# Performance work log

Measured on AMD Instinct MI355X. Metric: run time of the kernel, lower is better.

The kernel has to match this reference:

```python
import jax, jax.numpy as jnp
import numpy as np

D_MODEL = 512
D_FF = 512
N_EXPERTS = 16
TOP_K = 3
BATCH, SEQ = 1, 2048


def setup_inputs() -> dict:
    key = jax.random.key(0)
    ks = jax.random.split(key, 6)
    x = jax.random.normal(ks[0], (BATCH, SEQ, D_MODEL), dtype=jnp.float32)
    # router gate (std=0.01 per _init_weights)
    gate_w = 0.01 * jax.random.normal(ks[1], (N_EXPERTS, D_MODEL), dtype=jnp.float32)
    expert_bias = jnp.zeros((N_EXPERTS,), dtype=jnp.float32)  # registered buffer, zeros
    # shared SwiGLU expert (std=0.02)
    shared_gate_up = 0.02 * jax.random.normal(ks[2], (2 * D_FF, D_MODEL), dtype=jnp.float32)
    shared_down = 0.02 * jax.random.normal(ks[3], (D_MODEL, D_FF), dtype=jnp.float32)
    # batched routed experts (std=0.02)
    expert_gate_up = 0.02 * jax.random.normal(ks[4], (N_EXPERTS, 2 * D_FF, D_MODEL), dtype=jnp.float32)
    expert_down = 0.02 * jax.random.normal(ks[5], (N_EXPERTS, D_MODEL, D_FF), dtype=jnp.float32)
    return {
        "x": x,
        "gate_w": gate_w,
        "expert_bias": expert_bias,
        "shared_gate_up": shared_gate_up,
        "shared_down": shared_down,
        "expert_gate_up": expert_gate_up,
        "expert_down": expert_down,
    }


def _swiglu(combined):
    gate, up = jnp.split(combined, 2, axis=-1)
    return jax.nn.silu(gate) * up


def reference(x, gate_w, expert_bias, shared_gate_up, shared_down, expert_gate_up, expert_down):
    B, S, D = x.shape
    xf = x.reshape(-1, D)  # [T, D]

    # ---- shared expert (always active) ----
    shared_out = _swiglu(xf @ shared_gate_up.T) @ shared_down.T  # [T, D]

    # ---- router: sigmoid affinity + bias-adjusted top-k ----
    logits = xf @ gate_w.T  # [T, E]
    affinity = jax.nn.sigmoid(logits)
    routing_scores = affinity + expert_bias  # expert_bias buffer (zeros)
    _, sel = jax.lax.top_k(routing_scores, TOP_K)  # [T, K]
    sel_aff = jnp.take_along_axis(affinity, sel, axis=1)  # [T, K]
    gating = sel_aff / (sel_aff.sum(axis=-1, keepdims=True) + 1e-9)  # [T, K]

    # ---- routed experts: per-token SwiGLU with the token's expert weights ----
    # Computed densely per expert then gathered; identical math to the
    # per-token weight-gather in BatchedExperts.
    combined = jnp.einsum('td,efd->tef', xf, expert_gate_up)  # [T, E, 2F]
    hidden = _swiglu(combined)  # [T, E, F]
    expert_out = jnp.einsum('tef,edf->ted', hidden, expert_down)  # [T, E, D]
    sel_out = jnp.take_along_axis(expert_out, sel[:, :, None], axis=1)  # [T, K, D]
    routed_out = jnp.einsum('tk,tkd->td', gating, sel_out)  # [T, D]

    out = shared_out + routed_out  # dropout p=0.0 -> identity
    return out.reshape(B, S, D)
```

## Files before the change

kernel.cpp:

```cpp
#include <hip/hip_runtime.h>

#define T_TOK 2048
#define DM    512
#define DFF   512
#define NE    16
#define LDK   72

typedef __attribute__((ext_vector_type(8))) short bf16x8;
typedef __attribute__((ext_vector_type(4))) float f32x4;
typedef __attribute__((ext_vector_type(8))) unsigned short us8;

__device__ __forceinline__ unsigned short f2bf(float f) {
  unsigned int u = __float_as_uint(f);
  u += 0x7fffu + ((u >> 16) & 1u);
  return (unsigned short)(u >> 16);
}

__device__ __forceinline__ void cvt16(const float* __restrict__ p, us8* o) {
  float4 v0 = *(const float4*)(p);
  float4 v1 = *(const float4*)(p + 4);
  float4 v2 = *(const float4*)(p + 8);
  float4 v3 = *(const float4*)(p + 12);
  us8 a, b;
  a[0]=f2bf(v0.x); a[1]=f2bf(v0.y); a[2]=f2bf(v0.z); a[3]=f2bf(v0.w);
  a[4]=f2bf(v1.x); a[5]=f2bf(v1.y); a[6]=f2bf(v1.z); a[7]=f2bf(v1.w);
  b[0]=f2bf(v2.x); b[1]=f2bf(v2.y); b[2]=f2bf(v2.z); b[3]=f2bf(v2.w);
  b[4]=f2bf(v3.x); b[5]=f2bf(v3.y); b[6]=f2bf(v3.z); b[7]=f2bf(v3.w);
  o[0]=a; o[1]=b;
}

template<bool PRE>
__device__ __forceinline__ void stage16(const void* __restrict__ base, size_t off, us8* o) {
  if constexpr (PRE) {
    const unsigned short* p = (const unsigned short*)base + off;
    o[0] = *(const us8*)p;
    o[1] = *(const us8*)(p + 8);
  } else {
    cvt16((const float*)base + off, o);
  }
}

#define MFMA(a,b,c) __builtin_amdgcn_mfma_f32_16x16x32_bf16((a),(b),(c),0,0,0)

__global__ __launch_bounds__(256) void router_kernel(
    const float* __restrict__ x, const float* __restrict__ gw,
    const float* __restrict__ bias, int* __restrict__ counts,
    int* __restrict__ list, float* __restrict__ wgt)
{
  __shared__ float lg[4][16];
  __shared__ int bcnt[16], bbase[16];
  __shared__ int sel_s[4][3], pos_s[4][3];
  __shared__ float g_s[4][3];

  const int tid = threadIdx.x, w = tid >> 6, lane = tid & 63;
  if (tid < 16) bcnt[tid] = 0;
  const int tok = blockIdx.x * 4 + w;
  const int e = lane & 15, part = lane >> 4;

  const float* xr = x + (size_t)tok * DM + part * 128;
  const float* wr = gw + (size_t)e * DM + part * 128;
  float acc = 0.f;
  #pragma unroll 8
  for (int i = 0; i < 128; i += 4) {
    float4 xv = *(const float4*)(xr + i);
    float4 wv = *(const float4*)(wr + i);
    acc += xv.x*wv.x + xv.y*wv.y + xv.z*wv.z + xv.w*wv.w;
  }
  acc += __shfl_xor(acc, 16);
  acc += __shfl_xor(acc, 32);
  if (lane < 16) lg[w][lane] = 1.f / (1.f + __expf(-acc));
  __syncthreads();

  if (tid < 4) {
    float aff[16], sc[16];
    #pragma unroll
    for (int i = 0; i < 16; ++i) { aff[i] = lg[tid][i]; sc[i] = aff[i] + bias[i]; }
    int sel[3]; float sa[3]; float sum = 0.f;
    #pragma unroll
    for (int k = 0; k < 3; ++k) {
      float best = -1e30f; int bi = 0;
      for (int i = 0; i < 16; ++i) {
        bool used = false;
        for (int j = 0; j < k; ++j) used |= (sel[j] == i);
        if (!used && sc[i] > best) { best = sc[i]; bi = i; }
      }
      sel[k] = bi; sa[k] = aff[bi]; sum += aff[bi];
    }
    float inv = 1.f / (sum + 1e-9f);
    #pragma unroll
    for (int k = 0; k < 3; ++k) {
      int p = atomicAdd(&bcnt[sel[k]], 1);
      sel_s[tid][k] = sel[k]; pos_s[tid][k] = p; g_s[tid][k] = sa[k] * inv;
    }
  }
  __syncthreads();
  if (tid < 16) bbase[tid] = atomicAdd(&counts[tid], bcnt[tid]);
  __syncthreads();
  if (tid < 4) {
    #pragma unroll
    for (int k = 0; k < 3; ++k) {
      int E = sel_s[tid][k];
      int p = bbase[E] + pos_s[tid][k];
      list[E * T_TOK + p] = blockIdx.x * 4 + tid;
      wgt [E * T_TOK + p] = g_s[tid][k];
    }
  }
}

__global__ __launch_bounds__(256) void conv_kernel(
    const float* __restrict__ x,   const float* __restrict__ sgu,
    const float* __restrict__ sdn, const float* __restrict__ egu,
    const float* __restrict__ edn,
    unsigned short* __restrict__ xb,   unsigned short* __restrict__ sgub,
    unsigned short* __restrict__ sdnb, unsigned short* __restrict__ egub,
    unsigned short* __restrict__ ednb)
{
  int g = blockIdx.x * 256 + threadIdx.x;
  const float* s; unsigned short* d; int l;
  if      (g <  131072) { s = x;   d = xb;   l = g;           }
  else if (g <  196608) { s = sgu; d = sgub; l = g -  131072; }
  else if (g <  229376) { s = sdn; d = sdnb; l = g -  196608; }
  else if (g < 1277952) { s = egu; d = egub; l = g -  229376; }
  else                  { s = edn; d = ednb; l = g - 1277952; }
  const float* p = s + (size_t)l * 8;
  float4 v0 = *(const float4*)p;
  float4 v1 = *(const float4*)(p + 4);
  us8 o;
  o[0]=f2bf(v0.x); o[1]=f2bf(v0.y); o[2]=f2bf(v0.z); o[3]=f2bf(v0.w);
  o[4]=f2bf(v1.x); o[5]=f2bf(v1.y); o[6]=f2bf(v1.z); o[7]=f2bf(v1.w);
  *(us8*)(d + (size_t)l * 8) = o;
}

template<bool PRE>
__global__ __launch_bounds__(256) void gemm1_fused(
    const void* __restrict__ X, const void* __restrict__ Wsh,
    const void* __restrict__ Wex, unsigned short* __restrict__ Hall,
    const int* __restrict__ counts, const int* __restrict__ list)
{
  __shared__ unsigned short As[64][LDK];
  __shared__ unsigned short Bg[64][LDK];
  __shared__ unsigned short Bu[64][LDK];

  const int n0 = blockIdx.x * 64, mt = blockIdx.y, z = blockIdx.z;
  int cnt, hb; const void* W; size_t woff = 0;
  if (z == 0) { cnt = T_TOK; hb = 0; W = Wsh; }
  else {
    const int e = z - 1;
    cnt = counts[e];
    if (mt * 64 >= cnt) return;
    hb = T_TOK;
    for (int i = 0; i < e; ++i) hb += counts[i];
    W = Wex; woff = (size_t)e * (2 * DFF * DM);
  }

  const int tid = threadIdx.x;
  const int sr = tid >> 2;
  const int sc = (tid & 3) * 16;
  const int entry = mt * 64 + sr;
  const bool avalid = entry < cnt;
  size_t aoff = 0;
  if (avalid) {
    int tok = (z == 0) ? entry : list[(z - 1) * T_TOK + entry];
    aoff = (size_t)tok * DM;
  }
  const size_t goff = woff + (size_t)(n0 + sr) * DM;
  const size_t uoff = woff + (size_t)(DFF + n0 + sr) * DM;

  const int lane = tid & 63;
  const int wm = ((tid >> 6) & 1) * 32;
  const int wn = ((tid >> 7) & 1) * 32;
  const int lr = lane & 15;
  const int qd = lane >> 4;

  const f32x4 z4 = {0.f, 0.f, 0.f, 0.f};
  f32x4 accg[2][2], accu[2][2];
  #pragma unroll
  for (int i = 0; i < 2; ++i)
    #pragma unroll
    for (int j = 0; j < 2; ++j) { accg[i][j] = z4; accu[i][j] = z4; }

  for (int k0 = 0; k0 < DM; k0 += 64) {
    us8 av[2] = {{0,0,0,0,0,0,0,0},{0,0,0,0,0,0,0,0}};
    us8 gv[2], uv[2];
    if (avalid) stage16<PRE>(X, aoff + k0 + sc, av);
    stage16<PRE>(W, goff + k0 + sc, gv);
    stage16<PRE>(W, uoff + k0 + sc, uv);
    __syncthreads();
    *(us8*)&As[sr][sc] = av[0]; *(us8*)&As[sr][sc+8] = av[1];
    *(us8*)&Bg[sr][sc] = gv[0]; *(us8*)&Bg[sr][sc+8] = gv[1];
    *(us8*)&Bu[sr][sc] = uv[0]; *(us8*)&Bu[sr][sc+8] = uv[1];
    __syncthreads();
    #pragma unroll
    for (int ks = 0; ks < 2; ++ks) {
      const int kk = ks * 32 + qd * 8;
      bf16x8 a0 = *(const bf16x8*)&As[wm      + lr][kk];
      bf16x8 a1 = *(const bf16x8*)&As[wm + 16 + lr][kk];
      bf16x8 g0 = *(const bf16x8*)&Bg[wn      + lr][kk];
      bf16x8 g1 = *(const bf16x8*)&Bg[wn + 16 + lr][kk];
      bf16x8 u0 = *(const bf16x8*)&Bu[wn      + lr][kk];
      bf16x8 u1 = *(const bf16x8*)&Bu[wn + 16 + lr][kk];
      accg[0][0] = MFMA(a0, g0, accg[0][0]);
      accg[0][1] = MFMA(a0, g1, accg[0][1]);
      accg[1][0] = MFMA(a1, g0, accg[1][0]);
      accg[1][1] = MFMA(a1, g1, accg[1][1]);
      accu[0][0] = MFMA(a0, u0, accu[0][0]);
      accu[0][1] = MFMA(a0, u1, accu[0][1]);
      accu[1][0] = MFMA(a1, u0, accu[1][0]);
      accu[1][1] = MFMA(a1, u1, accu[1][1]);
    }
  }

  #pragma unroll
  for (int sm = 0; sm < 2; ++sm)
    #pragma unroll
    for (int sn = 0; sn < 2; ++sn) {
      const int col = n0 + wn + sn * 16 + lr;
      #pragma unroll
      for (int r = 0; r < 4; ++r) {
        const int ent = mt * 64 + wm + sm * 16 + qd * 4 + r;
        if (ent < cnt) {
          float g = accg[sm][sn][r];
          float u = accu[sm][sn][r];
          float h = (g / (1.f + __expf(-g))) * u;
          Hall[(size_t)(hb + ent) * DFF + col] = f2bf(h);
        }
      }
    }
}

template<bool PRE>
__global__ __launch_bounds__(256) void gemm2_fused(
    const unsigned short* __restrict__ Hall, const void* __restrict__ Wsh,
    const void* __restrict__ Wex, float* __restrict__ out,
    const int* __restrict__ counts, const int* __restrict__ list,
    const float* __restrict__ wgt)
{
  __shared__ unsigned short Ah[64][LDK];
  __shared__ unsigned short Bd[64][LDK];

  const int n0 = blockIdx.x * 64, mt = blockIdx.y, z = blockIdx.z;
  int cnt, hb; const void* W; size_t woff = 0;
  if (z == 0) { cnt = T_TOK; hb = 0; W = Wsh; }
  else {
    const int e = z - 1;
    cnt = counts[e];
    if (mt * 64 >= cnt) return;
    hb = T_TOK;
    for (int i = 0; i < e; ++i) hb += counts[i];
    W = Wex; woff = (size_t)e * (DM * DFF);
  }

  const int tid = threadIdx.x;
  const int sr = tid >> 2;
  const int sc = (tid & 3) * 16;
  const int entry = mt * 64 + sr;
  const bool avalid = entry < cnt;
  const unsigned short* arow = Hall;
  if (avalid) arow = Hall + (size_t)(hb + entry) * DFF;
  const size_t doff = woff + (size_t)(n0 + sr) * DFF;

  const int lane = tid & 63;
  const int wm = ((tid >> 6) & 1) * 32;
  const int wn = ((tid >> 7) & 1) * 32;
  const int lr = lane & 15;
  const int qd = lane >> 4;

  const f32x4 z4 = {0.f, 0.f, 0.f, 0.f};
  f32x4 acc[2][2];
  #pragma unroll
  for (int i = 0; i < 2; ++i)
    #pragma unroll
    for (int j = 0; j < 2; ++j) acc[i][j] = z4;

  for (int k0 = 0; k0 < DFF; k0 += 64) {
    us8 av0 = {0,0,0,0,0,0,0,0}, av1 = {0,0,0,0,0,0,0,0};
    if (avalid) {
      av0 = *(const us8*)(arow + k0 + sc);
      av1 = *(const us8*)(arow + k0 + sc + 8);
    }
    us8 dv[2];
    stage16<PRE>(W, doff + k0 + sc, dv);
    __syncthreads();
    *(us8*)&Ah[sr][sc] = av0;   *(us8*)&Ah[sr][sc+8] = av1;
    *(us8*)&Bd[sr][sc] = dv[0]; *(us8*)&Bd[sr][sc+8] = dv[1];
    __syncthreads();
    #pragma unroll
    for (int ks = 0; ks < 2; ++ks) {
      const int kk = ks * 32 + qd * 8;
      bf16x8 a0 = *(const bf16x8*)&Ah[wm      + lr][kk];
      bf16x8 a1 = *(const bf16x8*)&Ah[wm + 16 + lr][kk];
      bf16x8 b0 = *(const bf16x8*)&Bd[wn      + lr][kk];
      bf16x8 b1 = *(const bf16x8*)&Bd[wn + 16 + lr][kk];
      acc[0][0] = MFMA(a0, b0, acc[0][0]);
      acc[0][1] = MFMA(a0, b1, acc[0][1]);
      acc[1][0] = MFMA(a1, b0, acc[1][0]);
      acc[1][1] = MFMA(a1, b1, acc[1][1]);
    }
  }

  #pragma unroll
  for (int sm = 0; sm < 2; ++sm)
    #pragma unroll
    for (int sn = 0; sn < 2; ++sn) {
      const int col = n0 + wn + sn * 16 + lr;
      #pragma unroll
      for (int r = 0; r < 4; ++r) {
        const int ent = mt * 64 + wm + sm * 16 + qd * 4 + r;
        if (ent < cnt) {
          float v = acc[sm][sn][r];
          if (z == 0) {
            atomicAdd(out + (size_t)ent * DM + col, v);
          } else {
            int   tok = list[(z - 1) * T_TOK + ent];
            float g   = wgt [(z - 1) * T_TOK + ent];
            atomicAdd(out + (size_t)tok * DM + col, g * v);
          }
        }
      }
    }
}

extern "C" void kernel_launch(void* const* d_in, const int* in_sizes, int n_in,
                              void* d_out, int out_size, void* d_ws, size_t ws_size,
                              hipStream_t stream) {
  const float* x    = (const float*)d_in[0];
  const float* gw   = (const float*)d_in[1];
  const float* bias = (const float*)d_in[2];
  const float* sgu  = (const float*)d_in[3];
  const float* sdn  = (const float*)d_in[4];
  const float* egu  = (const float*)d_in[5];
  const float* edn  = (const float*)d_in[6];
  float* out = (float*)d_out;

  char* ws = (char*)d_ws;
  int*            counts = (int*)(ws + 0);
  int*            list   = (int*)(ws + 64);
  float*          wgt    = (float*)(ws + 131136);
  unsigned short* Hall   = (unsigned short*)(ws + 262208);
  unsigned short* xb   = (unsigned short*)(ws + 8650816);
  unsigned short* sgub = (unsigned short*)(ws + 10747968);
  unsigned short* sdnb = (unsigned short*)(ws + 11796544);
  unsigned short* egub = (unsigned short*)(ws + 12320832);
  unsigned short* ednb = (unsigned short*)(ws + 29098048);
  const size_t need_base = 8650816, need_pre = 37486656;
  if (ws_size < need_base) return;
  const bool pre = ws_size >= need_pre;

  hipMemsetAsync(counts, 0, 64, stream);
  hipMemsetAsync(out, 0, (size_t)out_size * sizeof(float), stream);
  router_kernel<<<512, 256, 0, stream>>>(x, gw, bias, counts, list, wgt);

  if (pre) {
    conv_kernel<<<7040, 256, 0, stream>>>(x, sgu, sdn, egu, edn,
                                          xb, sgub, sdnb, egub, ednb);
    gemm1_fused<true ><<<dim3(8, 32, NE + 1), 256, 0, stream>>>(xb, sgub, egub, Hall, counts, list);
    gemm2_fused<true ><<<dim3(8, 32, NE + 1), 256, 0, stream>>>(Hall, sdnb, ednb, out, counts, list, wgt);
  } else {
    gemm1_fused<false><<<dim3(8, 32, NE + 1), 256, 0, stream>>>(x, sgu, egu, Hall, counts, list);
    gemm2_fused<false><<<dim3(8, 32, NE + 1), 256, 0, stream>>>(Hall, sdn, edn, out, counts, list, wgt);
  }
}
```

Measured before the change: 184.1 us.

## Enlarge MoE GEMM tiles to 128x128 and fuse router with bf16 conversion

```diff
diff --git a/kernel.cpp b/kernel.cpp
--- a/kernel.cpp
+++ b/kernel.cpp
@@ -42,17 +42,44 @@
 
 #define MFMA(a,b,c) __builtin_amdgcn_mfma_f32_16x16x32_bf16((a),(b),(c),0,0,0)
 
-__global__ __launch_bounds__(256) void router_kernel(
+template<bool PRE>
+__global__ __launch_bounds__(256) void prep_kernel(
     const float* __restrict__ x, const float* __restrict__ gw,
     const float* __restrict__ bias, int* __restrict__ counts,
-    int* __restrict__ list, float* __restrict__ wgt)
+    int* __restrict__ list, float* __restrict__ wgt,
+    const float* __restrict__ sgu, const float* __restrict__ sdn,
+    const float* __restrict__ egu, const float* __restrict__ edn,
+    unsigned short* __restrict__ xb,   unsigned short* __restrict__ sgub,
+    unsigned short* __restrict__ sdnb, unsigned short* __restrict__ egub,
+    unsigned short* __restrict__ ednb)
 {
+  const int tid = threadIdx.x;
+  if (blockIdx.x >= 512) {
+    if constexpr (PRE) {
+      int g = (blockIdx.x - 512) * 256 + tid;
+      const float* s; unsigned short* d; int l;
+      if      (g <  131072) { s = x;   d = xb;   l = g;           }
+      else if (g <  196608) { s = sgu; d = sgub; l = g -  131072; }
+      else if (g <  229376) { s = sdn; d = sdnb; l = g -  196608; }
+      else if (g < 1277952) { s = egu; d = egub; l = g -  229376; }
+      else                  { s = edn; d = ednb; l = g - 1277952; }
+      const float* p = s + (size_t)l * 8;
+      float4 v0 = *(const float4*)p;
+      float4 v1 = *(const float4*)(p + 4);
+      us8 o;
+      o[0]=f2bf(v0.x); o[1]=f2bf(v0.y); o[2]=f2bf(v0.z); o[3]=f2bf(v0.w);
+      o[4]=f2bf(v1.x); o[5]=f2bf(v1.y); o[6]=f2bf(v1.z); o[7]=f2bf(v1.w);
+      *(us8*)(d + (size_t)l * 8) = o;
+    }
+    return;
+  }
+
   __shared__ float lg[4][16];
   __shared__ int bcnt[16], bbase[16];
   __shared__ int sel_s[4][3], pos_s[4][3];
   __shared__ float g_s[4][3];
 
-  const int tid = threadIdx.x, w = tid >> 6, lane = tid & 63;
+  const int w = tid >> 6, lane = tid & 63;
   if (tid < 16) bcnt[tid] = 0;
   const int tok = blockIdx.x * 4 + w;
   const int e = lane & 15, part = lane >> 4;
@@ -107,217 +134,212 @@
   }
 }
 
-__global__ __launch_bounds__(256) void conv_kernel(
-    const float* __restrict__ x,   const float* __restrict__ sgu,
-    const float* __restrict__ sdn, const float* __restrict__ egu,
-    const float* __restrict__ edn,
-    unsigned short* __restrict__ xb,   unsigned short* __restrict__ sgub,
-    unsigned short* __restrict__ sdnb, unsigned short* __restrict__ egub,
-    unsigned short* __restrict__ ednb)
-{
-  int g = blockIdx.x * 256 + threadIdx.x;
-  const float* s; unsigned short* d; int l;
-  if      (g <  131072) { s = x;   d = xb;   l = g;           }
-  else if (g <  196608) { s = sgu; d = sgub; l = g -  131072; }
-  else if (g <  229376) { s = sdn; d = sdnb; l = g -  196608; }
-  else if (g < 1277952) { s = egu; d = egub; l = g -  229376; }
-  else                  { s = edn; d = ednb; l = g - 1277952; }
-  const float* p = s + (size_t)l * 8;
-  float4 v0 = *(const float4*)p;
-  float4 v1 = *(const float4*)(p + 4);
-  us8 o;
-  o[0]=f2bf(v0.x); o[1]=f2bf(v0.y); o[2]=f2bf(v0.z); o[3]=f2bf(v0.w);
-  o[4]=f2bf(v1.x); o[5]=f2bf(v1.y); o[6]=f2bf(v1.z); o[7]=f2bf(v1.w);
-  *(us8*)(d + (size_t)l * 8) = o;
-}
-
 template<bool PRE>
-__global__ __launch_bounds__(256) void gemm1_fused(
+__global__ __launch_bounds__(256, 2) void gemm1_fused(
     const void* __restrict__ X, const void* __restrict__ Wsh,
     const void* __restrict__ Wex, unsigned short* __restrict__ Hall,
     const int* __restrict__ counts, const int* __restrict__ list)
 {
-  __shared__ unsigned short As[64][LDK];
-  __shared__ unsigned short Bg[64][LDK];
-  __shared__ unsigned short Bu[64][LDK];
-
-  const int n0 = blockIdx.x * 64, mt = blockIdx.y, z = blockIdx.z;
+  __shared__ unsigned short As[128][LDK];
+  __shared__ unsigned short Bs[256][LDK];
+
+  const int n0 = blockIdx.x * 128;
+  const int mt = blockIdx.y, z = blockIdx.z;
   int cnt, hb; const void* W; size_t woff = 0;
   if (z == 0) { cnt = T_TOK; hb = 0; W = Wsh; }
   else {
     const int e = z - 1;
     cnt = counts[e];
-    if (mt * 64 >= cnt) return;
+    if (mt * 128 >= cnt) return;
     hb = T_TOK;
     for (int i = 0; i < e; ++i) hb += counts[i];
     W = Wex; woff = (size_t)e * (2 * DFF * DM);
   }
 
   const int tid = threadIdx.x;
-  const int sr = tid >> 2;
-  const int sc = (tid & 3) * 16;
-  const int entry = mt * 64 + sr;
-  const bool avalid = entry < cnt;
+  const int ar = tid >> 1, ac = (tid & 1) * 32;
+  const int aent = mt * 128 + ar;
+  const bool aval = aent < cnt;
   size_t aoff = 0;
-  if (avalid) {
-    int tok = (z == 0) ? entry : list[(z - 1) * T_TOK + entry];
+  if (aval) {
+    const int tok = (z == 0) ? aent : list[(z - 1) * T_TOK + aent];
     aoff = (size_t)tok * DM;
   }
-  const size_t goff = woff + (size_t)(n0 + sr) * DM;
-  const size_t uoff = woff + (size_t)(DFF + n0 + sr) * DM;
-
-  const int lane = tid & 63;
-  const int wm = ((tid >> 6) & 1) * 32;
-  const int wn = ((tid >> 7) & 1) * 32;
-  const int lr = lane & 15;
-  const int qd = lane >> 4;
+  const int br = tid;
+  const size_t boff = woff +
+      (size_t)((br < 128) ? (n0 + br) : (DFF + n0 + (br - 128))) * DM;
+
+  const int w  = tid >> 6;
+  const int wm = (w & 1) * 64;
+  const int wh = (w >> 1) * 64;
+  const int lane = tid & 63, lr = lane & 15, qd = lane >> 4;
 
   const f32x4 z4 = {0.f, 0.f, 0.f, 0.f};
-  f32x4 accg[2][2], accu[2][2];
+  f32x4 accg[4][4], accu[4][4];
   #pragma unroll
-  for (int i = 0; i < 2; ++i)
-    #pragma unroll
-    for (int j = 0; j < 2; ++j) { accg[i][j] = z4; accu[i][j] = z4; }
+  for (int i = 0; i < 4; ++i)
+    #pragma unroll
+    for (int j = 0; j < 4; ++j) { accg[i][j] = z4; accu[i][j] = z4; }
 
   for (int k0 = 0; k0 < DM; k0 += 64) {
-    us8 av[2] = {{0,0,0,0,0,0,0,0},{0,0,0,0,0,0,0,0}};
-    us8 gv[2], uv[2];
-    if (avalid) stage16<PRE>(X, aoff + k0 + sc, av);
-    stage16<PRE>(W, goff + k0 + sc, gv);
-    stage16<PRE>(W, uoff + k0 + sc, uv);
+    us8 av[4] = {{0,0,0,0,0,0,0,0},{0,0,0,0,0,0,0,0},
+                 {0,0,0,0,0,0,0,0},{0,0,0,0,0,0,0,0}};
+    us8 bv[8];
+    if (aval) {
+      stage16<PRE>(X, aoff + k0 + ac,      av + 0);
+      stage16<PRE>(X, aoff + k0 + ac + 16, av + 2);
+    }
+    stage16<PRE>(W, boff + k0,      bv + 0);
+    stage16<PRE>(W, boff + k0 + 16, bv + 2);
+    stage16<PRE>(W, boff + k0 + 32, bv + 4);
+    stage16<PRE>(W, boff + k0 + 48, bv + 6);
     __syncthreads();
-    *(us8*)&As[sr][sc] = av[0]; *(us8*)&As[sr][sc+8] = av[1];
-    *(us8*)&Bg[sr][sc] = gv[0]; *(us8*)&Bg[sr][sc+8] = gv[1];
-    *(us8*)&Bu[sr][sc] = uv[0]; *(us8*)&Bu[sr][sc+8] = uv[1];
+    *(us8*)&As[ar][ac]      = av[0];
+    *(us8*)&As[ar][ac + 8]  = av[1];
+    *(us8*)&As[ar][ac + 16] = av[2];
+    *(us8*)&As[ar][ac + 24] = av[3];
+    #pragma unroll
+    for (int c = 0; c < 8; ++c) *(us8*)&Bs[br][c * 8] = bv[c];
     __syncthreads();
     #pragma unroll
     for (int ks = 0; ks < 2; ++ks) {
       const int kk = ks * 32 + qd * 8;
-      bf16x8 a0 = *(const bf16x8*)&As[wm      + lr][kk];
-      bf16x8 a1 = *(const bf16x8*)&As[wm + 16 + lr][kk];
-      bf16x8 g0 = *(const bf16x8*)&Bg[wn      + lr][kk];
-      bf16x8 g1 = *(const bf16x8*)&Bg[wn + 16 + lr][kk];
-      bf16x8 u0 = *(const bf16x8*)&Bu[wn      + lr][kk];
-      bf16x8 u1 = *(const bf16x8*)&Bu[wn + 16 + lr][kk];
-      accg[0][0] = MFMA(a0, g0, accg[0][0]);
-      accg[0][1] = MFMA(a0, g1, accg[0][1]);
-      accg[1][0] = MFMA(a1, g0, accg[1][0]);
-      accg[1][1] = MFMA(a1, g1, accg[1][1]);
-      accu[0][0] = MFMA(a0, u0, accu[0][0]);
-      accu[0][1] = MFMA(a0, u1, accu[0][1]);
-      accu[1][0] = MFMA(a1, u0, accu[1][0]);
-      accu[1][1] = MFMA(a1, u1, accu[1][1]);
+      bf16x8 a[4];
+      #pragma unroll
+      for (int i = 0; i < 4; ++i) a[i] = *(const bf16x8*)&As[wm + 16*i + lr][kk];
+      #pragma unroll
+      for (int j = 0; j < 4; ++j) {
+        bf16x8 bg = *(const bf16x8*)&Bs[      wh + 16*j + lr][kk];
+        bf16x8 bu = *(const bf16x8*)&Bs[128 + wh + 16*j + lr][kk];
+        #pragma unroll
+        for (int i = 0; i < 4; ++i) {
+          accg[i][j] = MFMA(a[i], bg, accg[i][j]);
+          accu[i][j] = MFMA(a[i], bu, accu[i][j]);
+        }
+      }
     }
   }
 
   #pragma unroll
-  for (int sm = 0; sm < 2; ++sm)
-    #pragma unroll
-    for (int sn = 0; sn < 2; ++sn) {
-      const int col = n0 + wn + sn * 16 + lr;
-      #pragma unroll
-      for (int r = 0; r < 4; ++r) {
-        const int ent = mt * 64 + wm + sm * 16 + qd * 4 + r;
-        if (ent < cnt) {
-          float g = accg[sm][sn][r];
-          float u = accu[sm][sn][r];
+  for (int i = 0; i < 4; ++i) {
+    #pragma unroll
+    for (int r = 0; r < 4; ++r) {
+      const int ent = mt * 128 + wm + 16 * i + qd * 4 + r;
+      if (ent < cnt) {
+        const size_t rowoff = (size_t)(hb + ent) * DFF + n0 + wh;
+        #pragma unroll
+        for (int j = 0; j < 4; ++j) {
+          float g = accg[i][j][r];
+          float u = accu[i][j][r];
           float h = (g / (1.f + __expf(-g))) * u;
-          Hall[(size_t)(hb + ent) * DFF + col] = f2bf(h);
+          Hall[rowoff + 16 * j + lr] = f2bf(h);
         }
       }
     }
+  }
 }
 
 template<bool PRE>
-__global__ __launch_bounds__(256) void gemm2_fused(
+__global__ __launch_bounds__(256, 2) void gemm2_fused(
     const unsigned short* __restrict__ Hall, const void* __restrict__ Wsh,
     const void* __restrict__ Wex, float* __restrict__ out,
     const int* __restrict__ counts, const int* __restrict__ list,
     const float* __restrict__ wgt)
 {
-  __shared__ unsigned short Ah[64][LDK];
-  __shared__ unsigned short Bd[64][LDK];
-
-  const int n0 = blockIdx.x * 64, mt = blockIdx.y, z = blockIdx.z;
+  __shared__ unsigned short Ah[128][LDK];
+  __shared__ unsigned short Bd[128][LDK];
+
+  const int n0 = blockIdx.x * 128;
+  const int mt = blockIdx.y, z = blockIdx.z;
   int cnt, hb; const void* W; size_t woff = 0;
   if (z == 0) { cnt = T_TOK; hb = 0; W = Wsh; }
   else {
     const int e = z - 1;
     cnt = counts[e];
-    if (mt * 64 >= cnt) return;
+    if (mt * 128 >= cnt) return;
     hb = T_TOK;
     for (int i = 0; i < e; ++i) hb += counts[i];
     W = Wex; woff = (size_t)e * (DM * DFF);
   }
 
   const int tid = threadIdx.x;
-  const int sr = tid >> 2;
-  const int sc = (tid & 3) * 16;
-  const int entry = mt * 64 + sr;
-  const bool avalid = entry < cnt;
-  const unsigned short* arow = Hall;
-  if (avalid) arow = Hall + (size_t)(hb + entry) * DFF;
-  const size_t doff = woff + (size_t)(n0 + sr) * DFF;
-
-  const int lane = tid & 63;
-  const int wm = ((tid >> 6) & 1) * 32;
-  const int wn = ((tid >> 7) & 1) * 32;
-  const int lr = lane & 15;
-  const int qd = lane >> 4;
+  const int ar = tid >> 1, ac = (tid & 1) * 32;
+  const int aent = mt * 128 + ar;
+  const bool aval = aent < cnt;
+  const size_t aoff = aval ? (size_t)(hb + aent) * DFF : 0;
+  const size_t boff = woff + (size_t)(n0 + ar) * DFF;
+
+  const int w  = tid >> 6;
+  const int wm = (w & 1) * 64;
+  const int wn = (w >> 1) * 64;
+  const int lane = tid & 63, lr = lane & 15, qd = lane >> 4;
 
   const f32x4 z4 = {0.f, 0.f, 0.f, 0.f};
-  f32x4 acc[2][2];
+  f32x4 acc[4][4];
   #pragma unroll
-  for (int i = 0; i < 2; ++i)
-    #pragma unroll
-    for (int j = 0; j < 2; ++j) acc[i][j] = z4;
+  for (int i = 0; i < 4; ++i)
+    #pragma unroll
+    for (int j = 0; j < 4; ++j) acc[i][j] = z4;
 
   for (int k0 = 0; k0 < DFF; k0 += 64) {
-    us8 av0 = {0,0,0,0,0,0,0,0}, av1 = {0,0,0,0,0,0,0,0};
-    if (avalid) {
-      av0 = *(const us8*)(arow + k0 + sc);
-      av1 = *(const us8*)(arow + k0 + sc + 8);
-    }
-    us8 dv[2];
-    stage16<PRE>(W, doff + k0 + sc, dv);
+    us8 av[4] = {{0,0,0,0,0,0,0,0},{0,0,0,0,0,0,0,0},
+                 {0,0,0,0,0,0,0,0},{0,0,0,0,0,0,0,0}};
+    us8 bv[4];
+    if (aval) {
+      av[0] = *(const us8*)(Hall + aoff + k0 + ac);
+      av[1] = *(const us8*)(Hall + aoff + k0 + ac + 8);
+      av[2] = *(const us8*)(Hall + aoff + k0 + ac + 16);
+      av[3] = *(const us8*)(Hall + aoff + k0 + ac + 24);
+    }
+    stage16<PRE>(W, boff + k0 + ac,      bv + 0);
+    stage16<PRE>(W, boff + k0 + ac + 16, bv + 2);
     __syncthreads();
-    *(us8*)&Ah[sr][sc] = av0;   *(us8*)&Ah[sr][sc+8] = av1;
-    *(us8*)&Bd[sr][sc] = dv[0]; *(us8*)&Bd[sr][sc+8] = dv[1];
+    *(us8*)&Ah[ar][ac]      = av[0];
+    *(us8*)&Ah[ar][ac + 8]  = av[1];
+    *(us8*)&Ah[ar][ac + 16] = av[2];
+    *(us8*)&Ah[ar][ac + 24] = av[3];
+    *(us8*)&Bd[ar][ac]      = bv[0];
+    *(us8*)&Bd[ar][ac + 8]  = bv[1];
+    *(us8*)&Bd[ar][ac + 16] = bv[2];
+    *(us8*)&Bd[ar][ac + 24] = bv[3];
     __syncthreads();
     #pragma unroll
     for (int ks = 0; ks < 2; ++ks) {
       const int kk = ks * 32 + qd * 8;
-      bf16x8 a0 = *(const bf16x8*)&Ah[wm      + lr][kk];
-      bf16x8 a1 = *(const bf16x8*)&Ah[wm + 16 + lr][kk];
-      bf16x8 b0 = *(const bf16x8*)&Bd[wn      + lr][kk];
-      bf16x8 b1 = *(const bf16x8*)&Bd[wn + 16 + lr][kk];
-      acc[0][0] = MFMA(a0, b0, acc[0][0]);
-      acc[0][1] = MFMA(a0, b1, acc[0][1]);
-      acc[1][0] = MFMA(a1, b0, acc[1][0]);
-      acc[1][1] = MFMA(a1, b1, acc[1][1]);
+      bf16x8 a[4];
+      #pragma unroll
+      for (int i = 0; i < 4; ++i) a[i] = *(const bf16x8*)&Ah[wm + 16*i + lr][kk];
+      #pragma unroll
+      for (int j = 0; j < 4; ++j) {
+        bf16x8 b = *(const bf16x8*)&Bd[wn + 16*j + lr][kk];
+        #pragma unroll
+        for (int i = 0; i < 4; ++i) acc[i][j] = MFMA(a[i], b, acc[i][j]);
+      }
     }
   }
 
   #pragma unroll
-  for (int sm = 0; sm < 2; ++sm)
-    #pragma unroll
-    for (int sn = 0; sn < 2; ++sn) {
-      const int col = n0 + wn + sn * 16 + lr;
-      #pragma unroll
-      for (int r = 0; r < 4; ++r) {
-        const int ent = mt * 64 + wm + sm * 16 + qd * 4 + r;
-        if (ent < cnt) {
-          float v = acc[sm][sn][r];
-          if (z == 0) {
-            atomicAdd(out + (size_t)ent * DM + col, v);
-          } else {
-            int   tok = list[(z - 1) * T_TOK + ent];
-            float g   = wgt [(z - 1) * T_TOK + ent];
-            atomicAdd(out + (size_t)tok * DM + col, g * v);
-          }
+  for (int i = 0; i < 4; ++i) {
+    #pragma unroll
+    for (int r = 0; r < 4; ++r) {
+      const int ent = mt * 128 + wm + 16 * i + qd * 4 + r;
+      if (ent < cnt) {
+        if (z == 0) {
+          float* orow = out + (size_t)ent * DM + n0 + wn;
+          #pragma unroll
+          for (int j = 0; j < 4; ++j)
+            atomicAdd(orow + 16 * j + lr, acc[i][j][r]);
+        } else {
+          const int   tok = list[(z - 1) * T_TOK + ent];
+          const float g   = wgt [(z - 1) * T_TOK + ent];
+          float* orow = out + (size_t)tok * DM + n0 + wn;
+          #pragma unroll
+          for (int j = 0; j < 4; ++j)
+            atomicAdd(orow + 16 * j + lr, g * acc[i][j][r]);
         }
       }
     }
+  }
 }
 
 extern "C" void kernel_launch(void* const* d_in, const int* in_sizes, int n_in,
@@ -348,15 +370,20 @@
 
   hipMemsetAsync(counts, 0, 64, stream);
   hipMemsetAsync(out, 0, (size_t)out_size * sizeof(float), stream);
-  router_kernel<<<512, 256, 0, stream>>>(x, gw, bias, counts, list, wgt);
 
   if (pre) {
-    conv_kernel<<<7040, 256, 0, stream>>>(x, sgu, sdn, egu, edn,
-                                          xb, sgub, sdnb, egub, ednb);
-    gemm1_fused<true ><<<dim3(8, 32, NE + 1), 256, 0, stream>>>(xb, sgub, egub, Hall, counts, list);
-    gemm2_fused<true ><<<dim3(8, 32, NE + 1), 256, 0, stream>>>(Hall, sdnb, ednb, out, counts, list, wgt);
+    prep_kernel<true><<<512 + 7040, 256, 0, stream>>>(
+        x, gw, bias, counts, list, wgt, sgu, sdn, egu, edn,
+        xb, sgub, sdnb, egub, ednb);
+    gemm1_fused<true ><<<dim3(4, 16, NE + 1), 256, 0, stream>>>(xb, sgub, egub, Hall, counts, list);
+    gemm2_fused<true ><<<dim3(4, 16, NE + 1), 256, 0, stream>>>(Hall, sdnb, ednb, out, counts, list, wgt);
   } else {
-    gemm1_fused<false><<<dim3(8, 32, NE + 1), 256, 0, stream>>>(x, sgu, egu, Hall, counts, list);
-    gemm2_fused<false><<<dim3(8, 32, NE + 1), 256, 0, stream>>>(Hall, sdn, edn, out, counts, list, wgt);
-  }
-}
+    prep_kernel<false><<<512, 256, 0, stream>>>(
+        x, gw, bias, counts, list, wgt, sgu, sdn, egu, edn,
+        (unsigned short*)nullptr, (unsigned short*)nullptr,
+        (unsigned short*)nullptr, (unsigned short*)nullptr,
+        (unsigned short*)nullptr);
+    gemm1_fused<false><<<dim3(4, 16, NE + 1), 256, 0, stream>>>(x, sgu, egu, Hall, counts, list);
+    gemm2_fused<false><<<dim3(4, 16, NE + 1), 256, 0, stream>>>(Hall, sdn, edn, out, counts, list, wgt);
+  }
+}
```

New measurement: 210.1 us. +14.1%, slower.
